# Performance work log

Measured on AMD Instinct MI355X. Metric: run time of the kernel, lower is better.

The kernel has to match this reference:

```python
import jax, jax.numpy as jnp
import numpy as np

DIM = 96          # adapter bottleneck dim
K = 3             # conv kernel size

def quick_gelu(x):
    return x * jax.nn.sigmoid(1.702 * x)

def setup_inputs() -> dict:
    key = jax.random.key(0)
    ks = jax.random.split(key, 12)
    B, H, W, C = 64, 28, 28, 384
    x   = jax.random.normal(ks[0], (B, H, W, C), jnp.float32)
    # adapter down/up (xavier-ish scale for down; up is zero-init in the
    # original but we use small random so gradients flow in tests)
    Wd  = jax.random.normal(ks[1], (C, DIM), jnp.float32) * 0.05
    bd  = jnp.zeros((DIM,), jnp.float32)
    Wu  = jax.random.normal(ks[2], (DIM, C), jnp.float32) * 0.02
    bu  = jnp.zeros((C,), jnp.float32)
    # meta_net: Linear(C,64) -> ReLU -> Linear(64,64)
    Wm1 = jax.random.normal(ks[3], (C, 64), jnp.float32) * 0.05
    bm1 = jnp.zeros((64,), jnp.float32)
    Wm2 = jax.random.normal(ks[4], (64, 64), jnp.float32) * 0.1
    bm2 = jnp.zeros((64,), jnp.float32)
    # conv hypernet: Linear(64, DIM*DIM*K*K)
    Wh  = jax.random.normal(ks[5], (64, DIM * DIM * K * K), jnp.float32) * 0.01
    bh  = jnp.zeros((DIM * DIM * K * K,), jnp.float32)
    # learned layer embedding
    emb = jax.random.normal(ks[6], (64,), jnp.float32)
    return {"x": x, "Wd": Wd, "bd": bd, "Wm1": Wm1, "bm1": bm1,
            "Wm2": Wm2, "bm2": bm2, "Wh": Wh, "bh": bh, "emb": emb,
            "Wu": Wu, "bu": bu}

def reference(x, Wd, bd, Wm1, bm1, Wm2, bm2, Wh, bh, emb, Wu, bu):
    B, H, W, C = x.shape
    # meta_net(x) then mean over spatial dims -> per-sample prompt feature [B,64]
    h = jax.nn.relu(jnp.einsum('bhwc,cd->bhwd', x, Wm1) + bm1)
    prompt = jnp.mean(jnp.einsum('bhwd,de->bhwe', h, Wm2) + bm2, axis=(1, 2))  # [B,64]
    # hypernet: per-sample dynamic conv weights (fuse_type='add')
    wflat = (emb[None, :] + prompt) @ Wh + bh                 # [B, DIM*DIM*9]
    wconv = wflat.reshape(B * DIM, DIM, K, K)                 # grouped OIHW
    # adapter down + QuickGELU
    xd = quick_gelu(jnp.einsum('bhwc,cd->bhwd', x, Wd) + bd)  # [B,H,W,DIM]
    # fused batched dynamic conv via grouped conv (groups = B)
    xg = xd.transpose(0, 3, 1, 2).reshape(1, B * DIM, H, W)   # [1,B*DIM,H,W]
    yg = jax.lax.conv_general_dilated(
        xg, wconv, window_strides=(1, 1), padding=((1, 1), (1, 1)),
        dimension_numbers=('NCHW', 'OIHW', 'NCHW'), feature_group_count=B)
    y = yg.reshape(B, DIM, H, W).transpose(0, 2, 3, 1)        # [B,H,W,DIM]
    y = quick_gelu(y)  # dropout is identity in eval mode
    return jnp.einsum('bhwd,dc->bhwc', y, Wu) + bu
```

## Files before the change

kernel.cpp:

```cpp
#include <hip/hip_runtime.h>
#include <hip/hip_fp16.h>

#define BATCH 64
#define HH    28
#define WW2   28
#define HWPX  784
#define PTOT  50176
#define CIN   384
#define DIM   96
#define MDIM  64
#define JTOT  82944
#define WSAMP 82944

#define XD_OFF 0u
#define Y_OFF  9633792u
#define WP_OFF 19267584u
#define HS_OFF 29884416u
#define Z_OFF  29900800u
#define WUT_OFF 29917184u

typedef _Float16 f16x8 __attribute__((ext_vector_type(8)));
typedef _Float16 f16x4 __attribute__((ext_vector_type(4)));
typedef float f32x4 __attribute__((ext_vector_type(4)));

__device__ __forceinline__ float qgelu(float v) {
    return v / (1.f + __expf(-1.702f * v));
}

__global__ void k0_wcvt(const float* __restrict__ Wm1,
                        const float* __restrict__ Wd,
                        const float* __restrict__ Wu,
                        _Float16* __restrict__ Wt,
                        _Float16* __restrict__ WuT)
{
    int i = blockIdx.x * 256 + threadIdx.x;
    if (i < 61440) {
        int o = i / CIN, k = i - o * CIN;
        float v = (o < MDIM) ? Wm1[k * MDIM + o] : Wd[k * DIM + (o - MDIM)];
        Wt[i] = (_Float16)v;
    } else {
        int j = i - 61440;
        int c = j / DIM, d = j - c * DIM;
        WuT[j] = (_Float16)Wu[d * CIN + c];
    }
}

__global__ __launch_bounds__(512, 4) void k1_mfma(
    const float* __restrict__ x, const _Float16* __restrict__ Wt,
    const float* __restrict__ bm1, const float* __restrict__ bd,
    float* __restrict__ hsum, __half* __restrict__ xd)
{
    __shared__ char smem[25088];
    _Float16* As  = (_Float16*)smem;
    _Float16* Bs  = (_Float16*)(smem + 10240);
    _Float16* xds = (_Float16*)smem;
    float*   hred = (float*)(smem + 24576);

    const int t = threadIdx.x;
    const int p0 = blockIdx.x * 128;
    const int lane = t & 63, w = t >> 6;
    const int wm = w >> 1, wn = w & 1;

    f32x4 acc[2][5];
    #pragma unroll
    for (int mf = 0; mf < 2; ++mf)
        #pragma unroll
        for (int nf = 0; nf < 5; ++nf) acc[mf][nf] = (f32x4){0.f, 0.f, 0.f, 0.f};

    float4 ra[2];
    uint4  rb0, rb1;
    const int ar0 = t >> 3, aq0 = t & 7;
    const int ar1 = (t + 512) >> 3, aq1 = t & 7;
    const int br0 = t >> 2, bq0 = t & 3;
    const int br1 = (t + 512) >> 2, bq1 = t & 3;

    {
        const int k0 = 0;
        ra[0] = *(const float4*)(x + (size_t)(p0 + ar0) * CIN + k0 + aq0 * 4);
        ra[1] = *(const float4*)(x + (size_t)(p0 + ar1) * CIN + k0 + aq1 * 4);
        rb0 = *(const uint4*)(Wt + br0 * CIN + k0 + bq0 * 8);
        if (t < 128) rb1 = *(const uint4*)(Wt + br1 * CIN + k0 + bq1 * 8);
    }

    for (int kc = 0; kc < 12; ++kc) {
        #pragma unroll
        for (int i = 0; i < 2; ++i) {
            const int r = i ? ar1 : ar0, q = i ? aq1 : aq0;
            f16x4 h;
            h[0] = (_Float16)ra[i].x; h[1] = (_Float16)ra[i].y;
            h[2] = (_Float16)ra[i].z; h[3] = (_Float16)ra[i].w;
            *(f16x4*)(As + r * 40 + q * 4) = h;
        }
        *(uint4*)(Bs + br0 * 40 + bq0 * 8) = rb0;
        if (t < 128) *(uint4*)(Bs + br1 * 40 + bq1 * 8) = rb1;
        __syncthreads();

        if (kc + 1 < 12) {
            const int k0 = (kc + 1) * 32;
            ra[0] = *(const float4*)(x + (size_t)(p0 + ar0) * CIN + k0 + aq0 * 4);
            ra[1] = *(const float4*)(x + (size_t)(p0 + ar1) * CIN + k0 + aq1 * 4);
            rb0 = *(const uint4*)(Wt + br0 * CIN + k0 + bq0 * 8);
            if (t < 128) rb1 = *(const uint4*)(Wt + br1 * CIN + k0 + bq1 * 8);
        }

        const int ko = (lane >> 4) * 8;
        const int rl = lane & 15;
        f16x8 av[2], bv[5];
        av[0] = *(f16x8*)(As + (wm * 32 + rl) * 40 + ko);
        av[1] = *(f16x8*)(As + (wm * 32 + 16 + rl) * 40 + ko);
        #pragma unroll
        for (int nf = 0; nf < 5; ++nf)
            bv[nf] = *(f16x8*)(Bs + (wn * 80 + nf * 16 + rl) * 40 + ko);
        #pragma unroll
        for (int mf = 0; mf < 2; ++mf)
            #pragma unroll
            for (int nf = 0; nf < 5; ++nf)
                acc[mf][nf] = __builtin_amdgcn_mfma_f32_16x16x32_f16(
                    av[mf], bv[nf], acc[mf][nf], 0, 0, 0);
        __syncthreads();
    }

    if (t < 128) hred[t] = 0.f;
    __syncthreads();

    const int s0 = p0 / HWPX, s_last = (p0 + 127) / HWPX;
    #pragma unroll
    for (int mf = 0; mf < 2; ++mf) {
        #pragma unroll
        for (int nf = 0; nf < 5; ++nf) {
            const int col = wn * 80 + nf * 16 + (lane & 15);
            #pragma unroll
            for (int j = 0; j < 4; ++j) {
                const int rl = wm * 32 + mf * 16 + (lane >> 4) * 4 + j;
                float v = acc[mf][nf][j];
                if (col < 64) {
                    v = fmaxf(v + bm1[col], 0.f);
                    int sloc = (p0 + rl) / HWPX - s0;
                    atomicAdd(&hred[sloc * 64 + col], v);
                } else {
                    int e = col - 64;
                    xds[rl * 96 + e] = (_Float16)qgelu(v + bd[e]);
                }
            }
        }
    }
    __syncthreads();

    if (t < 128) {
        int sloc = t >> 6, col = t & 63, s = s0 + sloc;
        if (s <= s_last) atomicAdd(&hsum[s * 64 + col], hred[t]);
    }
    #pragma unroll
    for (int i = 0; i < 3; ++i) {
        int e = t + i * 512;
        *(uint4*)((__half*)xd + (size_t)p0 * 96 + e * 8) = *(uint4*)(xds + e * 8);
    }
}

__global__ void k2a_prompt(const float* __restrict__ hsum,
                           const float* __restrict__ Wm2,
                           const float* __restrict__ bm2,
                           const float* __restrict__ emb,
                           float* __restrict__ z)
{
    int idx = blockIdx.x * 256 + threadIdx.x;
    int b = idx >> 6, m = idx & 63;
    float acc = 0.f;
    #pragma unroll 8
    for (int d = 0; d < 64; ++d) acc += hsum[b * 64 + d] * Wm2[d * 64 + m];
    z[idx] = emb[m] + acc * (1.f / 784.f) + bm2[m];
}

__global__ __launch_bounds__(256) void k2b_hyper(
    const float* __restrict__ z, const float* __restrict__ Wh,
    const float* __restrict__ bh, __half* __restrict__ wperm)
{
    __shared__ float  zs[4096];
    __shared__ __half wl[64 * 216];
    const int t = threadIdx.x;
    const int o = blockIdx.x >> 2, qd = blockIdx.x & 3;

    for (int idx = t; idx < 4096; idx += 256) zs[idx] = z[idx];

    const bool act = (t < 216);
    const int j = o * 864 + qd * 216 + (act ? t : 0);
    float wh[64];
    float bj = 0.f;
    if (act) {
        #pragma unroll 8
        for (int m = 0; m < 64; ++m) wh[m] = Wh[(size_t)m * JTOT + j];
        bj = bh[j];
    }
    __syncthreads();

    if (act) {
        const int il = t / 9, t9 = t - il * 9;
        const int loc = t9 * 24 + il;
        for (int b = 0; b < 64; ++b) {
            float a = bj;
            const float4* zz = (const float4*)(zs + b * 64);
            #pragma unroll
            for (int m4 = 0; m4 < 16; ++m4) {
                float4 v = zz[m4];
                a += v.x * wh[4 * m4] + v.y * wh[4 * m4 + 1] +
                     v.z * wh[4 * m4 + 2] + v.w * wh[4 * m4 + 3];
            }
            wl[b * 216 + loc] = __float2half(a);
        }
    }
    __syncthreads();

    for (int idx = t; idx < 3456; idx += 256) {
        int b = idx / 54, r = idx - b * 54;
        int t9 = r / 6, il4 = r - t9 * 6;
        *(uint2*)(wperm + (size_t)b * WSAMP + o * 864 + t9 * 96 + qd * 24 + il4 * 4) =
            *(const uint2*)(wl + b * 216 + t9 * 24 + il4 * 4);
    }
}

__global__ __launch_bounds__(256) void k3_mfma(
    const __half* __restrict__ xd, const __half* __restrict__ wperm,
    __half* __restrict__ y)
{
    __shared__ __half sm[17600];
    const int t = threadIdx.x;

    const int n = blockIdx.x;
    const int xcd = n & 7, jj0 = n >> 3;
    const int b = xcd * 8 + jj0 / 7;
    const int rt = jj0 % 7;
    const int h0 = rt * 4;

    if (t < 16) *(uint4*)(sm + 17472 + t * 8) = uint4{0u, 0u, 0u, 0u};
    for (int idx = t; idx < 2016; idx += 256) {
        int pix = idx / 12, q = idx - pix * 12;
        int r = pix / 28, col = pix - r * 28;
        int g = h0 - 1 + r;
        uint4 v = {0u, 0u, 0u, 0u};
        if ((unsigned)g < 28u)
            v = *(const uint4*)(xd + (size_t)(b * HWPX + g * 28 + col) * 96 + q * 8);
        *(uint4*)(sm + pix * 104 + q * 8) = v;
    }
    __syncthreads();

    const int lane = t & 63, w = t >> 6;
    const int wm = w >> 1, wn = w & 1;
    const int mloc = lane & 15, klo = (lane >> 4) * 8;
    const int base_m = wm * 64;

    int oh_[4], ow_[4]; bool pv[4];
    #pragma unroll
    for (int mf = 0; mf < 4; ++mf) {
        int p = base_m + mf * 16 + mloc;
        pv[mf] = (p < 112);
        int pp = pv[mf] ? p : 0;
        oh_[mf] = pp / 28; ow_[mf] = pp - oh_[mf] * 28;
    }
    const __half* wp = wperm + (size_t)b * WSAMP + (wn * 48 + mloc) * 864 + klo;

    f32x4 acc[4][3];
    #pragma unroll
    for (int mf = 0; mf < 4; ++mf)
        #pragma unroll
        for (int nf = 0; nf < 3; ++nf) acc[mf][nf] = (f32x4){0.f, 0.f, 0.f, 0.f};

    #pragma unroll
    for (int kh = 0; kh < 3; ++kh) {
        #pragma unroll
        for (int kw = 0; kw < 3; ++kw) {
            const int t9 = kh * 3 + kw;
            int abase[4];
            #pragma unroll
            for (int mf = 0; mf < 4; ++mf) {
                int iw = ow_[mf] + kw - 1;
                bool valid = pv[mf] && ((unsigned)iw < 28u);
                abase[mf] = valid ? ((oh_[mf] + kh) * 28 + iw) * 104 + klo
                                  : 17472 + klo;
            }
            #pragma unroll
            for (int ic = 0; ic < 3; ++ic) {
                f16x8 av[4], bv[3];
                #pragma unroll
                for (int nf = 0; nf < 3; ++nf)
                    bv[nf] = *(const f16x8*)(wp + nf * 13824 + t9 * 96 + ic * 32);
                #pragma unroll
                for (int mf = 0; mf < 4; ++mf)
                    av[mf] = *(const f16x8*)(sm + abase[mf] + ic * 32);
                #pragma unroll
                for (int mf = 0; mf < 4; ++mf)
                    #pragma unroll
                    for (int nf = 0; nf < 3; ++nf)
                        acc[mf][nf] = __builtin_amdgcn_mfma_f32_16x16x32_f16(
                            av[mf], bv[nf], acc[mf][nf], 0, 0, 0);
            }
        }
    }
    __syncthreads();

    #pragma unroll
    for (int mf = 0; mf < 4; ++mf) {
        #pragma unroll
        for (int nf = 0; nf < 3; ++nf) {
            const int o = wn * 48 + nf * 16 + mloc;
            #pragma unroll
            for (int j = 0; j < 4; ++j) {
                int p = base_m + mf * 16 + (lane >> 4) * 4 + j;
                if (p < 112)
                    sm[p * 104 + o] = __float2half(qgelu(acc[mf][nf][j]));
            }
        }
    }
    __syncthreads();
    for (int idx = t; idx < 1344; idx += 256) {
        int pix = idx / 12, q = idx - pix * 12;
        *(uint4*)(y + (size_t)(b * HWPX + h0 * 28 + pix) * 96 + q * 8) =
            *(uint4*)(sm + pix * 104 + q * 8);
    }
}

__global__ __launch_bounds__(512, 2) void k4_mfma(
    const __half* __restrict__ y, const _Float16* __restrict__ WuT,
    const float* __restrict__ bu, float* __restrict__ out)
{
    __shared__ __half ys[128 * 104];
    const int t = threadIdx.x;
    const int p0 = blockIdx.x * 128;

    #pragma unroll
    for (int i = 0; i < 3; ++i) {
        int idx = t + i * 512;
        int pix = idx / 12, q = idx - pix * 12;
        *(uint4*)(ys + pix * 104 + q * 8) =
            *(const uint4*)(y + (size_t)(p0 + pix) * 96 + q * 8);
    }

    const int lane = t & 63, w = t >> 6;
    const int wm = w >> 2, wn = w & 3;
    const int mloc = lane & 15, klo = (lane >> 4) * 8;

    float bcol[6];
    #pragma unroll
    for (int nf = 0; nf < 6; ++nf) bcol[nf] = bu[wn * 96 + nf * 16 + mloc];
    __syncthreads();

    f32x4 acc[4][6];
    #pragma unroll
    for (int mf = 0; mf < 4; ++mf)
        #pragma unroll
        for (int nf = 0; nf < 6; ++nf) acc[mf][nf] = (f32x4){0.f, 0.f, 0.f, 0.f};

    #pragma unroll
    for (int kc = 0; kc < 3; ++kc) {
        f16x8 av[4], bv[6];
        #pragma unroll
        for (int nf = 0; nf < 6; ++nf)
            bv[nf] = *(const f16x8*)(WuT + (wn * 96 + nf * 16 + mloc) * 96 + kc * 32 + klo);
        #pragma unroll
        for (int mf = 0; mf < 4; ++mf)
            av[mf] = *(const f16x8*)(ys + (wm * 64 + mf * 16 + mloc) * 104 + kc * 32 + klo);
        #pragma unroll
        for (int mf = 0; mf < 4; ++mf)
            #pragma unroll
            for (int nf = 0; nf < 6; ++nf)
                acc[mf][nf] = __builtin_amdgcn_mfma_f32_16x16x32_f16(
                    av[mf], bv[nf], acc[mf][nf], 0, 0, 0);
    }

    #pragma unroll
    for (int mf = 0; mf < 4; ++mf) {
        #pragma unroll
        for (int nf = 0; nf < 6; ++nf) {
            const int c = wn * 96 + nf * 16 + mloc;
            #pragma unroll
            for (int j = 0; j < 4; ++j) {
                int p = p0 + wm * 64 + mf * 16 + (lane >> 4) * 4 + j;
                out[(size_t)p * CIN + c] = acc[mf][nf][j] + bcol[nf];
            }
        }
    }
}

extern "C" void kernel_launch(void* const* d_in, const int* in_sizes, int n_in,
                              void* d_out, int out_size, void* d_ws, size_t ws_size,
                              hipStream_t stream)
{
    const float* x   = (const float*)d_in[0];
    const float* Wd  = (const float*)d_in[1];
    const float* bd  = (const float*)d_in[2];
    const float* Wm1 = (const float*)d_in[3];
    const float* bm1 = (const float*)d_in[4];
    const float* Wm2 = (const float*)d_in[5];
    const float* bm2 = (const float*)d_in[6];
    const float* Wh  = (const float*)d_in[7];
    const float* bh  = (const float*)d_in[8];
    const float* emb = (const float*)d_in[9];
    const float* Wu  = (const float*)d_in[10];
    const float* bu  = (const float*)d_in[11];
    float* out = (float*)d_out;

    char* ws = (char*)d_ws;
    __half*   xd    = (__half*)(ws + XD_OFF);
    __half*   ybuf  = (__half*)(ws + Y_OFF);
    __half*   wperm = (__half*)(ws + WP_OFF);
    float*    hsum  = (float*)(ws + HS_OFF);
    float*    z     = (float*)(ws + Z_OFF);
    _Float16* Wt    = (_Float16*)(ws + WP_OFF);
    _Float16* WuT   = (_Float16*)(ws + WUT_OFF);

    hipMemsetAsync(hsum, 0, 64 * 64 * sizeof(float), stream);

    k0_wcvt<<<384, 256, 0, stream>>>(Wm1, Wd, Wu, Wt, WuT);
    k1_mfma<<<392, 512, 0, stream>>>(x, Wt, bm1, bd, hsum, xd);
    k2a_prompt<<<16, 256, 0, stream>>>(hsum, Wm2, bm2, emb, z);
    k2b_hyper<<<384, 256, 0, stream>>>(z, Wh, bh, wperm);
    k3_mfma<<<448, 256, 0, stream>>>(xd, wperm, ybuf);
    k4_mfma<<<392, 512, 0, stream>>>(ybuf, WuT, bu, out);
}
```

Baseline: 141.5 us.

## Fuse dynamic conv and up-projection into one kernel, dropping the y buffer

New measurement: 149.8 us. 5.8% more time.

```diff
diff --git a/kernel.cpp b/kernel.cpp
--- a/kernel.cpp
+++ b/kernel.cpp
@@ -218,9 +218,10 @@
     }
 }
 
-__global__ __launch_bounds__(256) void k3_mfma(
+__global__ __launch_bounds__(256) void k34_convup(
     const __half* __restrict__ xd, const __half* __restrict__ wperm,
-    __half* __restrict__ y)
+    const _Float16* __restrict__ WuT, const float* __restrict__ bu,
+    float* __restrict__ out)
 {
     __shared__ __half sm[17600];
     const int t = threadIdx.x;
@@ -311,70 +312,48 @@
         }
     }
     __syncthreads();
-    for (int idx = t; idx < 1344; idx += 256) {
-        int pix = idx / 12, q = idx - pix * 12;
-        *(uint4*)(y + (size_t)(b * HWPX + h0 * 28 + pix) * 96 + q * 8) =
-            *(uint4*)(sm + pix * 104 + q * 8);
-    }
-}
-
-__global__ __launch_bounds__(512, 2) void k4_mfma(
-    const __half* __restrict__ y, const _Float16* __restrict__ WuT,
-    const float* __restrict__ bu, float* __restrict__ out)
-{
-    __shared__ __half ys[128 * 104];
-    const int t = threadIdx.x;
-    const int p0 = blockIdx.x * 128;
-
-    #pragma unroll
-    for (int i = 0; i < 3; ++i) {
-        int idx = t + i * 512;
-        int pix = idx / 12, q = idx - pix * 12;
-        *(uint4*)(ys + pix * 104 + q * 8) =
-            *(const uint4*)(y + (size_t)(p0 + pix) * 96 + q * 8);
-    }
-
-    const int lane = t & 63, w = t >> 6;
-    const int wm = w >> 2, wn = w & 3;
-    const int mloc = lane & 15, klo = (lane >> 4) * 8;
-
-    float bcol[6];
-    #pragma unroll
-    for (int nf = 0; nf < 6; ++nf) bcol[nf] = bu[wn * 96 + nf * 16 + mloc];
-    __syncthreads();
-
-    f32x4 acc[4][6];
-    #pragma unroll
-    for (int mf = 0; mf < 4; ++mf)
-        #pragma unroll
-        for (int nf = 0; nf < 6; ++nf) acc[mf][nf] = (f32x4){0.f, 0.f, 0.f, 0.f};
-
-    #pragma unroll
-    for (int kc = 0; kc < 3; ++kc) {
-        f16x8 av[4], bv[6];
-        #pragma unroll
-        for (int nf = 0; nf < 6; ++nf)
-            bv[nf] = *(const f16x8*)(WuT + (wn * 96 + nf * 16 + mloc) * 96 + kc * 32 + klo);
-        #pragma unroll
-        for (int mf = 0; mf < 4; ++mf)
-            av[mf] = *(const f16x8*)(ys + (wm * 64 + mf * 16 + mloc) * 104 + kc * 32 + klo);
-        #pragma unroll
-        for (int mf = 0; mf < 4; ++mf)
-            #pragma unroll
-            for (int nf = 0; nf < 6; ++nf)
-                acc[mf][nf] = __builtin_amdgcn_mfma_f32_16x16x32_f16(
-                    av[mf], bv[nf], acc[mf][nf], 0, 0, 0);
-    }
-
-    #pragma unroll
-    for (int mf = 0; mf < 4; ++mf) {
-        #pragma unroll
-        for (int nf = 0; nf < 6; ++nf) {
-            const int c = wn * 96 + nf * 16 + mloc;
-            #pragma unroll
-            for (int j = 0; j < 4; ++j) {
-                int p = p0 + wm * 64 + mf * 16 + (lane >> 4) * 4 + j;
-                out[(size_t)p * CIN + c] = acc[mf][nf][j] + bcol[nf];
+
+    const size_t rowbase = (size_t)(b * HWPX + h0 * 28);
+    const int qj = lane >> 4;
+    #pragma unroll
+    for (int cg = 0; cg < 2; ++cg) {
+        const int c0 = cg * 192 + w * 48;
+        float bc[3];
+        #pragma unroll
+        for (int nf = 0; nf < 3; ++nf) bc[nf] = bu[c0 + nf * 16 + mloc];
+
+        f32x4 a2[7][3];
+        #pragma unroll
+        for (int mf = 0; mf < 7; ++mf)
+            #pragma unroll
+            for (int nf = 0; nf < 3; ++nf) a2[mf][nf] = (f32x4){0.f, 0.f, 0.f, 0.f};
+
+        #pragma unroll
+        for (int kc = 0; kc < 3; ++kc) {
+            f16x8 bv2[3];
+            #pragma unroll
+            for (int nf = 0; nf < 3; ++nf)
+                bv2[nf] = *(const f16x8*)(WuT + (c0 + nf * 16 + mloc) * 96 + kc * 32 + klo);
+            #pragma unroll
+            for (int mf = 0; mf < 7; ++mf) {
+                f16x8 av2 = *(const f16x8*)(sm + (mf * 16 + mloc) * 104 + kc * 32 + klo);
+                #pragma unroll
+                for (int nf = 0; nf < 3; ++nf)
+                    a2[mf][nf] = __builtin_amdgcn_mfma_f32_16x16x32_f16(
+                        av2, bv2[nf], a2[mf][nf], 0, 0, 0);
+            }
+        }
+
+        #pragma unroll
+        for (int mf = 0; mf < 7; ++mf) {
+            #pragma unroll
+            for (int nf = 0; nf < 3; ++nf) {
+                const int c = c0 + nf * 16 + mloc;
+                #pragma unroll
+                for (int j = 0; j < 4; ++j) {
+                    int p = mf * 16 + qj * 4 + j;
+                    out[(rowbase + p) * CIN + c] = a2[mf][nf][j] + bc[nf];
+                }
             }
         }
     }
@@ -400,7 +379,6 @@
 
     char* ws = (char*)d_ws;
     __half*   xd    = (__half*)(ws + XD_OFF);
-    __half*   ybuf  = (__half*)(ws + Y_OFF);
     __half*   wperm = (__half*)(ws + WP_OFF);
     float*    hsum  = (float*)(ws + HS_OFF);
     float*    z     = (float*)(ws + Z_OFF);
@@ -413,6 +391,5 @@
     k1_mfma<<<392, 512, 0, stream>>>(x, Wt, bm1, bd, hsum, xd);
     k2a_prompt<<<16, 256, 0, stream>>>(hsum, Wm2, bm2, emb, z);
     k2b_hyper<<<384, 256, 0, stream>>>(z, Wh, bh, wperm);
-    k3_mfma<<<448, 256, 0, stream>>>(xd, wperm, ybuf);
-    k4_mfma<<<392, 512, 0, stream>>>(ybuf, WuT, bu, out);
-}
+    k34_convup<<<448, 256, 0, stream>>>(xd, wperm, WuT, bu, out);
+}
```
